# Kernel optimization log

Measured on AMD Instinct MI355X. Metric: run time of the kernel, lower is better.

Reference implementation:

```python
import jax, jax.numpy as jnp
import numpy as np

HIDDEN = 1024
HEADS = 8
HEAD_DIM = HIDDEN // HEADS  # 128
MAX_SEQ = 4096
MAX_TOKS = 2048
THETA = 10000.0
INIT_STD = 0.02


def setup_inputs() -> dict:
    key = jax.random.key(0)
    ks = jax.random.split(key, 8)
    B, L = 2, 4096
    hidden_states = jax.random.normal(ks[0], (B, L, HIDDEN), dtype=jnp.float32)
    attention_mask = jnp.ones((B, L), dtype=bool)
    segment_ids = jnp.sort(jax.random.randint(ks[1], (B, L), 0, 2), axis=-1).astype(jnp.int32)
    position_ids = jnp.sort(jax.random.randint(ks[2], (B, L), 0, MAX_SEQ), axis=-1).astype(jnp.int32)
    # nn.Linear weights stored (out_features, in_features), bias=False, normal(0, 0.02)
    wq = (jax.random.normal(ks[3], (HIDDEN, HIDDEN), dtype=jnp.float32) * INIT_STD)
    wk = (jax.random.normal(ks[4], (HIDDEN, HIDDEN), dtype=jnp.float32) * INIT_STD)
    wv = (jax.random.normal(ks[5], (HIDDEN, HIDDEN), dtype=jnp.float32) * INIT_STD)
    wo = (jax.random.normal(ks[6], (HIDDEN, HIDDEN), dtype=jnp.float32) * INIT_STD)
    return {
        "hidden_states": hidden_states,
        "wq": wq, "wk": wk, "wv": wv, "wo": wo,
        "attention_mask": attention_mask,
        "segment_ids": segment_ids,
        "position_ids": position_ids,
    }


def _freqs_cis(position_ids):
    # precompute_freqs_cis gathered at position_ids -> (B, L, HEAD_DIM//2) complex
    inv_freq = 1.0 / (THETA ** (jnp.arange(0, HEAD_DIM, 2, dtype=jnp.float32) / HEAD_DIM))
    ang = position_ids.astype(jnp.float32)[..., None] * inv_freq  # (B,L,D/2)
    return jax.lax.complex(jnp.cos(ang), jnp.sin(ang))


def _apply_rope(x, fc):
    # x: (B,L,H,D); fc: (B,L,D/2) complex; broadcast fc over heads
    xs = x.astype(jnp.float32).reshape(*x.shape[:-1], HEAD_DIM // 2, 2)
    xc = jax.lax.complex(xs[..., 0], xs[..., 1])  # (B,L,H,D/2)
    out = xc * fc[:, :, None, :]
    return jnp.stack([jnp.real(out), jnp.imag(out)], axis=-1).reshape(x.shape).astype(x.dtype)


def reference(hidden_states, wq, wk, wv, wo, attention_mask, segment_ids, position_ids):
    B, L, _ = hidden_states.shape
    q = (hidden_states @ wq.T).reshape(B, L, HEADS, HEAD_DIM)
    k = (hidden_states @ wk.T).reshape(B, L, HEADS, HEAD_DIM)
    v = (hidden_states @ wv.T).reshape(B, L, HEADS, HEAD_DIM)

    fc = _freqs_cis(position_ids)
    q = _apply_rope(q, fc)
    k = _apply_rope(k, fc)

    # block-causal mask: query block index >= key block index
    blk = jnp.arange(L) // MAX_TOKS
    causal = blk[:, None] >= blk[None, :]                                   # (L,L)
    seg = (segment_ids[:, :, None] == segment_ids[:, None, :])              # (B,L,L)
    mask = attention_mask[:, None, None, :] & seg[:, None, :, :] & causal[None, None, :, :]

    scale = 1.0 / np.float32(np.sqrt(HEAD_DIM))
    scores = jnp.einsum('bqhd,bkhd->bhqk', q, k) * scale                    # (B,H,L,L)
    scores = jnp.where(mask, scores, jnp.float32(-jnp.inf))
    probs = jax.nn.softmax(scores, axis=-1)
    attn = jnp.einsum('bhqk,bkhd->bqhd', probs, v).reshape(B, L, HIDDEN)
    return attn @ wo.T
```

## Files before the change

kernel.cpp:

```cpp
#include <hip/hip_runtime.h>
#include <hip/hip_bf16.h>
#include <cstdint>
#include <cstddef>
#include <type_traits>

#define HID 1024
#define HEADS 8
#define HDIM 128
#define SEQ 4096
#define BATCH 2

typedef float f32x4 __attribute__((ext_vector_type(4)));
typedef float f32x16 __attribute__((ext_vector_type(16)));
typedef short bf16x8 __attribute__((ext_vector_type(8)));
typedef unsigned short u16x8 __attribute__((ext_vector_type(8)));

typedef bf16x8 __attribute__((may_alias)) bf16x8_a;
typedef u16x8  __attribute__((may_alias)) u16x8_a;
typedef float4 __attribute__((may_alias)) float4_a;
typedef unsigned int __attribute__((may_alias)) u32_a;

__device__ __forceinline__ unsigned short f2bf(float f) {
    union { float f; unsigned int u; } v; v.f = f;
    unsigned int u = v.u;
    unsigned int r = (u + 0x7FFFu + ((u >> 16) & 1u)) >> 16;
    return (unsigned short)r;
}
__device__ __forceinline__ float bf2f(unsigned short h) {
    union { unsigned int u; float f; } v; v.u = ((unsigned int)h) << 16;
    return v.f;
}

__device__ __forceinline__ void plane_swap(unsigned int& x, unsigned int& y) {
    asm("v_permlane32_swap_b32 %0, %1" : "+v"(x), "+v"(y));
}
__device__ __forceinline__ unsigned int cvt_pk(float lo, float hi) {
    unsigned int r;
    asm("v_cvt_pk_bf16_f32 %0, %1, %2" : "=v"(r) : "v"(lo), "v"(hi));
    return r;
}
__device__ __forceinline__ bf16x8 pack4(unsigned int a, unsigned int b,
                                        unsigned int c, unsigned int d) {
    union { unsigned int u[4]; bf16x8 v; } t;
    t.u[0] = a; t.u[1] = b; t.u[2] = c; t.u[3] = d;
    return t.v;
}
__device__ __forceinline__ void g2lds16(const unsigned short* g, unsigned short* l) {
    __builtin_amdgcn_global_load_lds(
        (const __attribute__((address_space(1))) void*)g,
        (__attribute__((address_space(3))) void*)l, 16, 0, 0);
}

__global__ __launch_bounds__(256)
void cvt_kernel(const float* __restrict__ X, unsigned short* __restrict__ Y)
{
    int i = (blockIdx.x * 256 + threadIdx.x) * 8;
    float4 d0 = *(const float4_a*)&X[i];
    float4 d1 = *(const float4_a*)&X[i + 4];
    u16x8 t;
    t[0] = f2bf(d0.x); t[1] = f2bf(d0.y); t[2] = f2bf(d0.z); t[3] = f2bf(d0.w);
    t[4] = f2bf(d1.x); t[5] = f2bf(d1.y); t[6] = f2bf(d1.z); t[7] = f2bf(d1.w);
    *(u16x8_a*)&Y[i] = t;
}

__global__ __launch_bounds__(256)
void cvtw_kernel(const float* __restrict__ w0, const float* __restrict__ w1,
                 const float* __restrict__ w2, const float* __restrict__ w3,
                 unsigned short* __restrict__ Y)
{
    const int WSZ8 = (HID * HID) / 8;
    int c = blockIdx.x * 256 + threadIdx.x;
    int quarter = c >> 17;
    int idx = (c & (WSZ8 - 1)) * 8;
    const float* w = quarter == 0 ? w0 : quarter == 1 ? w1 : quarter == 2 ? w2 : w3;
    float4 d0 = *(const float4_a*)&w[idx];
    float4 d1 = *(const float4_a*)&w[idx + 4];
    u16x8 t;
    t[0] = f2bf(d0.x); t[1] = f2bf(d0.y); t[2] = f2bf(d0.z); t[3] = f2bf(d0.w);
    t[4] = f2bf(d1.x); t[5] = f2bf(d1.y); t[6] = f2bf(d1.z); t[7] = f2bf(d1.w);
    *(u16x8_a*)&Y[(size_t)quarter * HID * HID + idx] = t;
}

template<typename OutT>
__global__ __launch_bounds__(256)
void gemm_swz(const unsigned short* __restrict__ A, const unsigned short* __restrict__ B,
              OutT* __restrict__ C, int M, int N, int K, int lda)
{
    __shared__ __align__(16) unsigned short Al[128][64];
    __shared__ __align__(16) unsigned short Bl[128][64];
    const int tid  = threadIdx.x;
    const int lane = tid & 63;
    const int w    = tid >> 6;
    const int wr   = w >> 1, wc = w & 1;
    const int l16  = lane & 15, l4 = lane >> 4;
    const int tm   = blockIdx.y * 128, tn = blockIdx.x * 128;
    const int srow  = lane >> 3;
    const int sslot = (lane & 7) ^ srow;

    f32x4 acc[4][4] = {};

    for (int ko = 0; ko < K; ko += 64) {
        __syncthreads();
#pragma unroll
        for (int it = 0; it < 4; ++it) {
            int ca = w * 4 + it;
            int row = ca * 8 + srow;
            g2lds16(&A[(size_t)(tm + row) * lda + ko + sslot * 8], &Al[ca * 8][0]);
            g2lds16(&B[(size_t)(tn + row) * K   + ko + sslot * 8], &Bl[ca * 8][0]);
        }
        __syncthreads();
#pragma unroll
        for (int kk = 0; kk < 2; ++kk) {
            const int rslot = (kk * 4 + l4) ^ (l16 & 7);
            bf16x8 af[4], bfr[4];
#pragma unroll
            for (int i = 0; i < 4; ++i)
                af[i] = *(const bf16x8_a*)&Al[wr*64 + i*16 + l16][rslot * 8];
#pragma unroll
            for (int j = 0; j < 4; ++j)
                bfr[j] = *(const bf16x8_a*)&Bl[wc*64 + j*16 + l16][rslot * 8];
#pragma unroll
            for (int i = 0; i < 4; ++i)
#pragma unroll
                for (int j = 0; j < 4; ++j)
                    acc[i][j] = __builtin_amdgcn_mfma_f32_16x16x32_bf16(af[i], bfr[j], acc[i][j], 0, 0, 0);
        }
    }
#pragma unroll
    for (int i = 0; i < 4; ++i)
#pragma unroll
        for (int j = 0; j < 4; ++j)
#pragma unroll
            for (int r = 0; r < 4; ++r) {
                int row = tm + wr*64 + i*16 + l4*4 + r;
                int col = tn + wc*64 + j*16 + l16;
                if constexpr (std::is_same<OutT, float>::value)
                    C[(size_t)row * N + col] = acc[i][j][r];
                else
                    C[(size_t)row * N + col] = f2bf(acc[i][j][r]);
            }
}

template<bool A_BF16, bool B_BF16, typename OutT>
__global__ __launch_bounds__(256)
void gemm_bt(const void* __restrict__ Av, const void* __restrict__ Bv,
             OutT* __restrict__ C, int M, int N, int K, int lda)
{
    __shared__ __align__(16) unsigned short Al[128][72];
    __shared__ __align__(16) unsigned short Bl[128][72];
    const int tid  = threadIdx.x;
    const int lane = tid & 63;
    const int w    = tid >> 6;
    const int wr   = w >> 1, wc = w & 1;
    const int l16  = lane & 15, l4 = lane >> 4;
    const int tm   = blockIdx.y * 128, tn = blockIdx.x * 128;

    f32x4 acc[4][4] = {};

    for (int ko = 0; ko < K; ko += 64) {
        __syncthreads();
#pragma unroll
        for (int it = 0; it < 4; ++it) {
            int c = tid + 256 * it;
            int row = c >> 3, col0 = (c & 7) * 8;
            if constexpr (A_BF16) {
                const unsigned short* A = (const unsigned short*)Av;
                *(u16x8_a*)&Al[row][col0] =
                    *(const u16x8_a*)&A[(size_t)(tm + row) * lda + ko + col0];
            } else {
                const float* A = (const float*)Av;
                const float* p = &A[(size_t)(tm + row) * lda + ko + col0];
                float4 d0 = *(const float4_a*)p;
                float4 d1 = *(const float4_a*)(p + 4);
                u16x8 t;
                t[0] = f2bf(d0.x); t[1] = f2bf(d0.y); t[2] = f2bf(d0.z); t[3] = f2bf(d0.w);
                t[4] = f2bf(d1.x); t[5] = f2bf(d1.y); t[6] = f2bf(d1.z); t[7] = f2bf(d1.w);
                *(u16x8_a*)&Al[row][col0] = t;
            }
            if constexpr (B_BF16) {
                const unsigned short* B = (const unsigned short*)Bv;
                *(u16x8_a*)&Bl[row][col0] =
                    *(const u16x8_a*)&B[(size_t)(tn + row) * K + ko + col0];
            } else {
                const float* B = (const float*)Bv;
                const float* p = &B[(size_t)(tn + row) * K + ko + col0];
                float4 d0 = *(const float4_a*)p;
                float4 d1 = *(const float4_a*)(p + 4);
                u16x8 t;
                t[0] = f2bf(d0.x); t[1] = f2bf(d0.y); t[2] = f2bf(d0.z); t[3] = f2bf(d0.w);
                t[4] = f2bf(d1.x); t[5] = f2bf(d1.y); t[6] = f2bf(d1.z); t[7] = f2bf(d1.w);
                *(u16x8_a*)&Bl[row][col0] = t;
            }
        }
        __syncthreads();
#pragma unroll
        for (int kk = 0; kk < 2; ++kk) {
            bf16x8 af[4], bfr[4];
#pragma unroll
            for (int i = 0; i < 4; ++i)
                af[i] = *(const bf16x8_a*)&Al[wr*64 + i*16 + l16][kk*32 + l4*8];
#pragma unroll
            for (int j = 0; j < 4; ++j)
                bfr[j] = *(const bf16x8_a*)&Bl[wc*64 + j*16 + l16][kk*32 + l4*8];
#pragma unroll
            for (int i = 0; i < 4; ++i)
#pragma unroll
                for (int j = 0; j < 4; ++j)
                    acc[i][j] = __builtin_amdgcn_mfma_f32_16x16x32_bf16(af[i], bfr[j], acc[i][j], 0, 0, 0);
        }
    }
#pragma unroll
    for (int i = 0; i < 4; ++i)
#pragma unroll
        for (int j = 0; j < 4; ++j)
#pragma unroll
            for (int r = 0; r < 4; ++r) {
                int row = tm + wr*64 + i*16 + l4*4 + r;
                int col = tn + wc*64 + j*16 + l16;
                if constexpr (std::is_same<OutT, float>::value)
                    C[(size_t)row * N + col] = acc[i][j][r];
                else
                    C[(size_t)row * N + col] = f2bf(acc[i][j][r]);
            }
}

template<int NH>
__global__ __launch_bounds__(256)
void rope_kernel(unsigned short* __restrict__ X, const int* __restrict__ pos_ids, int RS)
{
    int c = blockIdx.x * 256 + threadIdx.x;
    int d0 = (c & 15) * 8;
    int l  = (c >> 4) & 4095;
    int b  = c >> 16;
    int pos = pos_ids[b * SEQ + l];
    float sth[4], cth[4];
#pragma unroll
    for (int j = 0; j < 4; ++j) {
        int i = (d0 >> 1) + j;
        float invf = powf(10000.0f, -(float)i * (1.0f / 64.0f));
        float ang = (float)pos * invf;
        sincosf(ang, &sth[j], &cth[j]);
    }
    size_t base = (size_t)(b * SEQ + l) * RS + d0;
#pragma unroll
    for (int h = 0; h < NH; ++h) {
        u16x8 d = *(const u16x8_a*)&X[base + h * HDIM];
#pragma unroll
        for (int j = 0; j < 4; ++j) {
            float x0 = bf2f(d[2*j]), x1 = bf2f(d[2*j+1]);
            d[2*j]   = f2bf(x0 * cth[j] - x1 * sth[j]);
            d[2*j+1] = f2bf(x0 * sth[j] + x1 * cth[j]);
        }
        *(u16x8_a*)&X[base + h * HDIM] = d;
    }
}

__global__ __launch_bounds__(256, 2)
void attn_kernel(const unsigned short* Q,
                 const unsigned short* K,
                 const unsigned short* V,
                 const int* __restrict__ seg,
                 unsigned short* O, int RS)
{
    __shared__ __align__(16) unsigned short Kl[2][64][136];
    __shared__ __align__(16) unsigned short Vt[2][128][72];

    const int tid  = threadIdx.x;
    const int lane = tid & 63;
    const int l32  = lane & 31, hi = lane >> 5;
    const int w    = tid >> 6;
    const int qt = (SEQ / 128 - 1) - blockIdx.x;
    const int h  = blockIdx.y;
    const int b  = blockIdx.z;
    const int qg0 = qt * 128 + w * 32;
    const int hoff = h * HDIM;

    bf16x8 qf[8];
    {
        size_t base = (size_t)(b * SEQ + qg0 + l32) * RS + hoff;
#pragma unroll
        for (int kk = 0; kk < 8; ++kk)
            qf[kk] = *(const bf16x8_a*)&Q[base + kk*16 + hi*8];
    }

    f32x16 acco0 = {}, acco1 = {}, acco2 = {}, acco3 = {};
    float lsum = 0.f;

    const int nkt = ((qt >> 4) + 1) * 32;

    int lo = 0, hb = SEQ;
    while (lo < hb) { int mid = (lo + hb) >> 1; if (seg[b * SEQ + mid] == 0) lo = mid + 1; else hb = mid; }
    const int boundary = lo;
    const bool blk_seg1 = (seg[b * SEQ + qt * 128] == 1);
    const bool blk_seg0 = (seg[b * SEQ + qt * 128 + 127] == 0);
    const bool mixed = !blk_seg0 && !blk_seg1;
    int kstart = 0, kend = nkt;
    if (blk_seg1) kstart = boundary >> 6;
    if (blk_seg0) {
        int ke = (boundary + 63) >> 6;
        kend = ke < nkt ? ke : nkt;
    }
    const bool qlt = (qg0 + l32) < boundary;

    const int kp = tid & 31, db = tid >> 5;
    const float sc = 0.08838834764831845f;

    u16x8 kreg[4], v0a, v0b, v1a, v1b;
    {
        const int kb = kstart * 64;
#pragma unroll
        for (int it = 0; it < 4; ++it) {
            int c = tid + 256 * it;
            kreg[it] = *(const u16x8_a*)&K[(size_t)(b * SEQ + kb + (c >> 4)) * RS + hoff + (c & 15) * 8];
        }
        size_t vb0 = (size_t)(b * SEQ + kb + 2 * kp) * RS + hoff + db * 16;
        size_t vb1 = (size_t)(b * SEQ + kb + 2 * kp + 1) * RS + hoff + db * 16;
        v0a = *(const u16x8_a*)&V[vb0];     v0b = *(const u16x8_a*)&V[vb0 + 8];
        v1a = *(const u16x8_a*)&V[vb1];     v1b = *(const u16x8_a*)&V[vb1 + 8];
    }
#pragma unroll
    for (int it = 0; it < 4; ++it) {
        int c = tid + 256 * it;
        *(u16x8_a*)&Kl[0][c >> 4][(c & 15) * 8] = kreg[it];
    }
#pragma unroll
    for (int j = 0; j < 8; ++j) {
        *(u32_a*)&Vt[0][db * 16 + j][2 * kp] =
            (unsigned int)(unsigned short)v0a[j] | ((unsigned int)(unsigned short)v1a[j] << 16);
        *(u32_a*)&Vt[0][db * 16 + 8 + j][2 * kp] =
            (unsigned int)(unsigned short)v0b[j] | ((unsigned int)(unsigned short)v1b[j] << 16);
    }
    if (kstart + 1 < kend) {
        const int kb2 = (kstart + 1) * 64;
#pragma unroll
        for (int it = 0; it < 4; ++it) {
            int c = tid + 256 * it;
            kreg[it] = *(const u16x8_a*)&K[(size_t)(b * SEQ + kb2 + (c >> 4)) * RS + hoff + (c & 15) * 8];
        }
        size_t vb0 = (size_t)(b * SEQ + kb2 + 2 * kp) * RS + hoff + db * 16;
        size_t vb1 = (size_t)(b * SEQ + kb2 + 2 * kp + 1) * RS + hoff + db * 16;
        v0a = *(const u16x8_a*)&V[vb0];     v0b = *(const u16x8_a*)&V[vb0 + 8];
        v1a = *(const u16x8_a*)&V[vb1];     v1b = *(const u16x8_a*)&V[vb1 + 8];
    }
    __syncthreads();

    int buf = 0;
    for (int kt = kstart; kt < kend; ++kt) {
        const int kb = kt * 64;

        f32x16 a0 = {}, a1 = {};
#pragma unroll
        for (int kk = 0; kk < 8; ++kk) {
            bf16x8 k0 = *(const bf16x8_a*)&Kl[buf][     l32][kk*16 + hi*8];
            bf16x8 k1 = *(const bf16x8_a*)&Kl[buf][32 + l32][kk*16 + hi*8];
            a0 = __builtin_amdgcn_mfma_f32_32x32x16_bf16(k0, qf[kk], a0, 0, 0, 0);
            a1 = __builtin_amdgcn_mfma_f32_32x32x16_bf16(k1, qf[kk], a1, 0, 0, 0);
        }

        unsigned int pk0[8], pk1[8];
        const bool need_mask = mixed || (kb < boundary && kb + 64 > boundary);
        if (need_mask) {
            const int kb0 = kb + 4 * hi, kb1 = kb + 32 + 4 * hi;
#pragma unroll
            for (int i = 0; i < 8; ++i) {
                int r0 = 2 * i;
                int off = (r0 & 3) + 8 * (r0 >> 2);
                float p0 = ((kb0 + off     < boundary) == qlt) ? __expf(a0[r0]     * sc) : 0.0f;
                float p1 = ((kb0 + off + 1 < boundary) == qlt) ? __expf(a0[r0 + 1] * sc) : 0.0f;
                float q0 = ((kb1 + off     < boundary) == qlt) ? __expf(a1[r0]     * sc) : 0.0f;
                float q1 = ((kb1 + off + 1 < boundary) == qlt) ? __expf(a1[r0 + 1] * sc) : 0.0f;
                lsum += (p0 + p1) + (q0 + q1);
                pk0[i] = cvt_pk(p0, p1);
                pk1[i] = cvt_pk(q0, q1);
            }
        } else {
#pragma unroll
            for (int i = 0; i < 8; ++i) {
                int r0 = 2 * i;
                float p0 = __expf(a0[r0]     * sc);
                float p1 = __expf(a0[r0 + 1] * sc);
                float q0 = __expf(a1[r0]     * sc);
                float q1 = __expf(a1[r0 + 1] * sc);
                lsum += (p0 + p1) + (q0 + q1);
                pk0[i] = cvt_pk(p0, p1);
                pk1[i] = cvt_pk(q0, q1);
            }
        }
        plane_swap(pk0[0], pk0[2]); plane_swap(pk0[1], pk0[3]);
        plane_swap(pk0[4], pk0[6]); plane_swap(pk0[5], pk0[7]);
        plane_swap(pk1[0], pk1[2]); plane_swap(pk1[1], pk1[3]);
        plane_swap(pk1[4], pk1[6]); plane_swap(pk1[5], pk1[7]);
        bf16x8 pf[4];
        pf[0] = pack4(pk0[0], pk0[1], pk0[2], pk0[3]);
        pf[1] = pack4(pk0[4], pk0[5], pk0[6], pk0[7]);
        pf[2] = pack4(pk1[0], pk1[1], pk1[2], pk1[3]);
        pf[3] = pack4(pk1[4], pk1[5], pk1[6], pk1[7]);

#pragma unroll
        for (int ks = 0; ks < 4; ++ks) {
            bf16x8 vf0 = *(const bf16x8_a*)&Vt[buf][      l32][ks*16 + hi*8];
            bf16x8 vf1 = *(const bf16x8_a*)&Vt[buf][32  + l32][ks*16 + hi*8];
            bf16x8 vf2 = *(const bf16x8_a*)&Vt[buf][64  + l32][ks*16 + hi*8];
            bf16x8 vf3 = *(const bf16x8_a*)&Vt[buf][96  + l32][ks*16 + hi*8];
            acco0 = __builtin_amdgcn_mfma_f32_32x32x16_bf16(pf[ks], vf0, acco0, 0, 0, 0);
            acco1 = __builtin_amdgcn_mfma_f32_32x32x16_bf16(pf[ks], vf1, acco1, 0, 0, 0);
            acco2 = __builtin_amdgcn_mfma_f32_32x32x16_bf16(pf[ks], vf2, acco2, 0, 0, 0);
            acco3 = __builtin_amdgcn_mfma_f32_32x32x16_bf16(pf[ks], vf3, acco3, 0, 0, 0);
        }

        if (kt + 1 < kend) {
            const int nb = buf ^ 1;
#pragma unroll
            for (int it = 0; it < 4; ++it) {
                int c = tid + 256 * it;
                *(u16x8_a*)&Kl[nb][c >> 4][(c & 15) * 8] = kreg[it];
            }
#pragma unroll
            for (int j = 0; j < 8; ++j) {
                *(u32_a*)&Vt[nb][db * 16 + j][2 * kp] =
                    (unsigned int)(unsigned short)v0a[j] | ((unsigned int)(unsigned short)v1a[j] << 16);
                *(u32_a*)&Vt[nb][db * 16 + 8 + j][2 * kp] =
                    (unsigned int)(unsigned short)v0b[j] | ((unsigned int)(unsigned short)v1b[j] << 16);
            }
            if (kt + 2 < kend) {
                const int kb2 = (kt + 2) * 64;
#pragma unroll
                for (int it = 0; it < 4; ++it) {
                    int c = tid + 256 * it;
                    kreg[it] = *(const u16x8_a*)&K[(size_t)(b * SEQ + kb2 + (c >> 4)) * RS + hoff + (c & 15) * 8];
                }
                size_t vb0 = (size_t)(b * SEQ + kb2 + 2 * kp) * RS + hoff + db * 16;
                size_t vb1 = (size_t)(b * SEQ + kb2 + 2 * kp + 1) * RS + hoff + db * 16;
                v0a = *(const u16x8_a*)&V[vb0];     v0b = *(const u16x8_a*)&V[vb0 + 8];
                v1a = *(const u16x8_a*)&V[vb1];     v1b = *(const u16x8_a*)&V[vb1 + 8];
            }
            __syncthreads();
        }
        buf ^= 1;
    }

    float tot = lsum + __shfl_xor(lsum, 32, 64);
#pragma unroll
    for (int r = 0; r < 16; ++r) {
        int qrow = (r & 3) + 8 * (r >> 2) + 4 * hi;
        float inv = 1.0f / __shfl(tot, qrow, 64);
        size_t base = (size_t)(b * SEQ + qg0 + qrow) * RS + hoff;
        O[base +       l32] = f2bf(acco0[r] * inv);
        O[base +  32 + l32] = f2bf(acco1[r] * inv);
        O[base +  64 + l32] = f2bf(acco2[r] * inv);
        O[base +  96 + l32] = f2bf(acco3[r] * inv);
    }
}

extern "C" void kernel_launch(void* const* d_in, const int* in_sizes, int n_in,
                              void* d_out, int out_size, void* d_ws, size_t ws_size,
                              hipStream_t stream)
{
    const float* X  = (const float*)d_in[0];
    const float* wq = (const float*)d_in[1];
    const float* wk = (const float*)d_in[2];
    const float* wv = (const float*)d_in[3];
    const float* wo = (const float*)d_in[4];
    const int* seg = (const int*)d_in[n_in - 2];
    const int* pos = (const int*)d_in[n_in - 1];
    float* out = (float*)d_out;

    const size_t NTOK = (size_t)BATCH * SEQ;
    const size_t MAT  = NTOK * HID;
    const size_t WSZ  = (size_t)HID * HID;

    if (ws_size >= (4 * MAT + 4 * WSZ) * sizeof(unsigned short)) {
        unsigned short* QKVb = (unsigned short*)d_ws;
        unsigned short* Xb   = QKVb + 3 * MAT;
        unsigned short* Wb   = Xb + MAT;
        unsigned short* Wob  = Wb + 3 * WSZ;

        cvt_kernel<<<(int)(MAT / (256 * 8)), 256, 0, stream>>>(X, Xb);
        cvtw_kernel<<<(int)(4 * WSZ / (256 * 8)), 256, 0, stream>>>(wq, wk, wv, wo, Wb);

        dim3 gq(3 * HID / 128, (int)(NTOK / 128));
        gemm_swz<unsigned short><<<gq, 256, 0, stream>>>(
            Xb, Wb, QKVb, (int)NTOK, 3 * HID, HID, HID);

        rope_kernel<16><<<(BATCH * SEQ * 16) / 256, 256, 0, stream>>>(QKVb, pos, 3 * HID);

        dim3 ga(SEQ / 128, HEADS, BATCH);
        attn_kernel<<<ga, 256, 0, stream>>>(QKVb, QKVb + HID, QKVb + 2 * HID, seg,
                                            QKVb , 3 * HID);

        dim3 go(HID / 128, (int)(NTOK / 128));
        gemm_swz<float><<<go, 256, 0, stream>>>(
            QKVb, Wob, out, (int)NTOK, HID, HID, 3 * HID);
    } else {
        unsigned short* Qb = (unsigned short*)d_ws;
        unsigned short* Kb = Qb + MAT;
        unsigned short* Vb = Kb + MAT;

        dim3 gg(HID / 128, (int)(NTOK / 128));
        gemm_bt<false, false, unsigned short><<<gg, 256, 0, stream>>>(
            (const void*)X, (const void*)wq, Qb, (int)NTOK, HID, HID, HID);
        gemm_bt<false, false, unsigned short><<<gg, 256, 0, stream>>>(
            (const void*)X, (const void*)wk, Kb, (int)NTOK, HID, HID, HID);
        gemm_bt<false, false, unsigned short><<<gg, 256, 0, stream>>>(
            (const void*)X, (const void*)wv, Vb, (int)NTOK, HID, HID, HID);

        rope_kernel<8><<<(BATCH * SEQ * 16) / 256, 256, 0, stream>>>(Qb, pos, HID);
        rope_kernel<8><<<(BATCH * SEQ * 16) / 256, 256, 0, stream>>>(Kb, pos, HID);

        dim3 ga(SEQ / 128, HEADS, BATCH);
        attn_kernel<<<ga, 256, 0, stream>>>(Qb, Kb, Vb, seg, Qb, HID);

        gemm_bt<true, false, float><<<gg, 256, 0, stream>>>(
            (const void*)Qb, (const void*)wo, out, (int)NTOK, HID, HID, HID);
    }
}
```

Measured before the change: 204.3 us.

## Swizzle GEMM tile order, use exp2, raise MFMA priority, move LDS stores earlier

The GEMM kernel now remaps block IDs with an XCD-style interleave (id&7 stride) so neighbouring tiles share L2 on each chiplet. In attention, exp is computed as exp2 with the log2e factor folded into the scale, which saves a multiply per element. The MFMA loops are bracketed with s_setprio so MFMA-issuing waves get scheduling priority. The stores of the next K/V tile into LDS are moved to right after the QK MFMAs, so they overlap with the softmax ALU work instead of following the PV MFMAs. The swizzle assumes the block count divides by eight to stay a valid permutation.

```diff
diff --git a/kernel.cpp b/kernel.cpp
--- a/kernel.cpp
+++ b/kernel.cpp
@@ -93,7 +93,11 @@
     const int w    = tid >> 6;
     const int wr   = w >> 1, wc = w & 1;
     const int l16  = lane & 15, l4 = lane >> 4;
-    const int tm   = blockIdx.y * 128, tn = blockIdx.x * 128;
+    const int nwg  = gridDim.x * gridDim.y;
+    const int id   = blockIdx.y * gridDim.x + blockIdx.x;
+    const int swz  = (id & 7) * (nwg >> 3) + (id >> 3);
+    const int bx   = swz % gridDim.x, by = swz / gridDim.x;
+    const int tm   = by * 128, tn = bx * 128;
     const int srow  = lane >> 3;
     const int sslot = (lane & 7) ^ srow;
 
@@ -303,7 +307,7 @@
     const bool qlt = (qg0 + l32) < boundary;
 
     const int kp = tid & 31, db = tid >> 5;
-    const float sc = 0.08838834764831845f;
+    const float sc2 = 0.08838834764831845f * 1.4426950408889634f;
 
     u16x8 kreg[4], v0a, v0b, v1a, v1b;
     {
@@ -347,8 +351,10 @@
     int buf = 0;
     for (int kt = kstart; kt < kend; ++kt) {
         const int kb = kt * 64;
+        const bool have_next = (kt + 1 < kend);
 
         f32x16 a0 = {}, a1 = {};
+        __builtin_amdgcn_s_setprio(1);
 #pragma unroll
         for (int kk = 0; kk < 8; ++kk) {
             bf16x8 k0 = *(const bf16x8_a*)&Kl[buf][     l32][kk*16 + hi*8];
@@ -356,6 +362,23 @@
             a0 = __builtin_amdgcn_mfma_f32_32x32x16_bf16(k0, qf[kk], a0, 0, 0, 0);
             a1 = __builtin_amdgcn_mfma_f32_32x32x16_bf16(k1, qf[kk], a1, 0, 0, 0);
         }
+        __builtin_amdgcn_s_setprio(0);
+
+        if (have_next) {
+            const int nb = buf ^ 1;
+#pragma unroll
+            for (int it = 0; it < 4; ++it) {
+                int c = tid + 256 * it;
+                *(u16x8_a*)&Kl[nb][c >> 4][(c & 15) * 8] = kreg[it];
+            }
+#pragma unroll
+            for (int j = 0; j < 8; ++j) {
+                *(u32_a*)&Vt[nb][db * 16 + j][2 * kp] =
+                    (unsigned int)(unsigned short)v0a[j] | ((unsigned int)(unsigned short)v1a[j] << 16);
+                *(u32_a*)&Vt[nb][db * 16 + 8 + j][2 * kp] =
+                    (unsigned int)(unsigned short)v0b[j] | ((unsigned int)(unsigned short)v1b[j] << 16);
+            }
+        }
 
         unsigned int pk0[8], pk1[8];
         const bool need_mask = mixed || (kb < boundary && kb + 64 > boundary);
@@ -365,10 +388,10 @@
             for (int i = 0; i < 8; ++i) {
                 int r0 = 2 * i;
                 int off = (r0 & 3) + 8 * (r0 >> 2);
-                float p0 = ((kb0 + off     < boundary) == qlt) ? __expf(a0[r0]     * sc) : 0.0f;
-                float p1 = ((kb0 + off + 1 < boundary) == qlt) ? __expf(a0[r0 + 1] * sc) : 0.0f;
-                float q0 = ((kb1 + off     < boundary) == qlt) ? __expf(a1[r0]     * sc) : 0.0f;
-                float q1 = ((kb1 + off + 1 < boundary) == qlt) ? __expf(a1[r0 + 1] * sc) : 0.0f;
+                float p0 = ((kb0 + off     < boundary) == qlt) ? exp2f(a0[r0]     * sc2) : 0.0f;
+                float p1 = ((kb0 + off + 1 < boundary) == qlt) ? exp2f(a0[r0 + 1] * sc2) : 0.0f;
+                float q0 = ((kb1 + off     < boundary) == qlt) ? exp2f(a1[r0]     * sc2) : 0.0f;
+                float q1 = ((kb1 + off + 1 < boundary) == qlt) ? exp2f(a1[r0 + 1] * sc2) : 0.0f;
                 lsum += (p0 + p1) + (q0 + q1);
                 pk0[i] = cvt_pk(p0, p1);
                 pk1[i] = cvt_pk(q0, q1);
@@ -377,10 +400,10 @@
 #pragma unroll
             for (int i = 0; i < 8; ++i) {
                 int r0 = 2 * i;
-                float p0 = __expf(a0[r0]     * sc);
-                float p1 = __expf(a0[r0 + 1] * sc);
-                float q0 = __expf(a1[r0]     * sc);
-                float q1 = __expf(a1[r0 + 1] * sc);
+                float p0 = exp2f(a0[r0]     * sc2);
+                float p1 = exp2f(a0[r0 + 1] * sc2);
+                float q0 = exp2f(a1[r0]     * sc2);
+                float q1 = exp2f(a1[r0 + 1] * sc2);
                 lsum += (p0 + p1) + (q0 + q1);
                 pk0[i] = cvt_pk(p0, p1);
                 pk1[i] = cvt_pk(q0, q1);
@@ -396,6 +419,7 @@
         pf[2] = pack4(pk1[0], pk1[1], pk1[2], pk1[3]);
         pf[3] = pack4(pk1[4], pk1[5], pk1[6], pk1[7]);
 
+        __builtin_amdgcn_s_setprio(1);
 #pragma unroll
         for (int ks = 0; ks < 4; ++ks) {
             bf16x8 vf0 = *(const bf16x8_a*)&Vt[buf][      l32][ks*16 + hi*8];
@@ -407,21 +431,9 @@
             acco2 = __builtin_amdgcn_mfma_f32_32x32x16_bf16(pf[ks], vf2, acco2, 0, 0, 0);
             acco3 = __builtin_amdgcn_mfma_f32_32x32x16_bf16(pf[ks], vf3, acco3, 0, 0, 0);
         }
-
-        if (kt + 1 < kend) {
-            const int nb = buf ^ 1;
-#pragma unroll
-            for (int it = 0; it < 4; ++it) {
-                int c = tid + 256 * it;
-                *(u16x8_a*)&Kl[nb][c >> 4][(c & 15) * 8] = kreg[it];
-            }
-#pragma unroll
-            for (int j = 0; j < 8; ++j) {
-                *(u32_a*)&Vt[nb][db * 16 + j][2 * kp] =
-                    (unsigned int)(unsigned short)v0a[j] | ((unsigned int)(unsigned short)v1a[j] << 16);
-                *(u32_a*)&Vt[nb][db * 16 + 8 + j][2 * kp] =
-                    (unsigned int)(unsigned short)v0b[j] | ((unsigned int)(unsigned short)v1b[j] << 16);
-            }
+        __builtin_amdgcn_s_setprio(0);
+
+        if (have_next) {
             if (kt + 2 < kend) {
                 const int kb2 = (kt + 2) * 64;
 #pragma unroll
```

New measurement: 211.1 us. 3.3% more time.
